# Performance work log

Measured on AMD Instinct MI355X. Metric: run time of the kernel, lower is better.

Reference implementation:

```python
import jax, jax.numpy as jnp
import numpy as np

NUM_HEADS = 16


def _qdq(x):
    """Symmetric int8 fake-quant along the last axis (per-token for
    activations, per-output-channel for [out,in] weights). Equivalent math to
    int8 GEMM with dynamic scales: (x_q @ w_q.T) * sx * sw == qdq(x) @ qdq(w).T."""
    s = jnp.maximum(jnp.max(jnp.abs(x), axis=-1, keepdims=True) / 127.0, 1e-8)
    return jnp.clip(jnp.round(x / s), -127.0, 127.0) * s


def setup_inputs() -> dict:
    key = jax.random.key(0)
    ks = jax.random.split(key, 8)
    B, N, M, D = 2, 4096, 512, 2048
    w_std = 0.02
    return {
        "x": jax.random.normal(ks[0], (B, N, D), jnp.float32),
        "cond": jax.random.normal(ks[1], (B, M, D), jnp.float32),
        "wq": jax.random.normal(ks[2], (D, D), jnp.float32) * w_std,
        "bq": jax.random.normal(ks[3], (D,), jnp.float32) * w_std,
        "wkv": jax.random.normal(ks[4], (2 * D, D), jnp.float32) * w_std,
        "bkv": jax.random.normal(ks[5], (2 * D,), jnp.float32) * w_std,
        "wp": jax.random.normal(ks[6], (D, D), jnp.float32) * w_std,
        "bp": jax.random.normal(ks[7], (D,), jnp.float32) * w_std,
    }


def reference(x, cond, wq, bq, wkv, bkv, wp, bp):
    B, N, C = x.shape
    M = cond.shape[1]
    H = NUM_HEADS
    Dh = C // H

    # W8A8 dynamic-scale q projection (per-token act quant, per-channel weight quant)
    q = _qdq(x) @ _qdq(wq).T + bq                      # [B,N,C]
    # fp16-style kv projection
    kv = cond @ wkv.T + bkv                            # [B,M,2C]
    k, v = jnp.split(kv, 2, axis=-1)                   # view(...,2,H,Dh).unbind(2)

    q = q.reshape(B, N, H, Dh)
    k = k.reshape(B, M, H, Dh)
    v = v.reshape(B, M, H, Dh)

    scale = 1.0 / np.sqrt(Dh)
    attn = jax.nn.softmax(jnp.einsum('bnhd,bmhd->bhnm', q, k) * scale, axis=-1)
    o = jnp.einsum('bhnm,bmhd->bnhd', attn, v).reshape(B, N, C)

    # fused quant_sum (per-token requant of attention output) + W8A8 proj
    out = _qdq(o) @ _qdq(wp).T + bp                    # [B,N,C]
    return out
```

## Files before the change

kernel.cpp:

```cpp
#include <hip/hip_runtime.h>
#include <cstdint>
#include <cstddef>


typedef __bf16 bf16_t;
typedef __bf16 bf16x8 __attribute__((ext_vector_type(8)));
typedef float f32x4 __attribute__((ext_vector_type(4)));

__device__ __forceinline__ void gld16(void* lds, const void* g) {
    __builtin_amdgcn_global_load_lds(
        (__attribute__((address_space(1))) uint32_t*)(uintptr_t)g,
        (__attribute__((address_space(3))) uint32_t*)(uint32_t)(uintptr_t)lds,
        16, 0, 0);
}

__device__ __forceinline__ void load8(const float* p, int i, float* v) {
    const float4* p4 = (const float4*)p;
    float4 a = p4[2 * i], b = p4[2 * i + 1];
    v[0] = a.x; v[1] = a.y; v[2] = a.z; v[3] = a.w;
    v[4] = b.x; v[5] = b.y; v[6] = b.z; v[7] = b.w;
}
__device__ __forceinline__ void load8(const bf16_t* p, int i, float* v) {
    bf16x8 t = ((const bf16x8*)p)[i];
#pragma unroll
    for (int j = 0; j < 8; ++j) v[j] = (float)t[j];
}

template <int QUANT, typename T>
__global__ __launch_bounds__(256) void rowpack(const T* __restrict__ in,
                                               bf16_t* __restrict__ out, int K) {
    const int tid = threadIdx.x;
    const size_t row = blockIdx.x;
    const T* rp = in + row * (size_t)K;
    const int n8 = K >> 3;
    float scale = 1.0f;
    if (QUANT) {
        float m = 0.f;
        for (int i = tid; i < n8; i += 256) {
            float v[8];
            load8(rp, i, v);
#pragma unroll
            for (int j = 0; j < 8; ++j) m = fmaxf(m, fabsf(v[j]));
        }
        __shared__ float red[256];
        red[tid] = m;
        __syncthreads();
        for (int s = 128; s > 0; s >>= 1) {
            if (tid < s) red[tid] = fmaxf(red[tid], red[tid + s]);
            __syncthreads();
        }
        scale = fmaxf(red[0] * (1.0f / 127.0f), 1e-8f);
    }
    const int KT = K >> 5;
    const int p = (int)(row >> 7), c = ((int)row >> 4) & 7, lm = (int)row & 15;
    for (int i = tid; i < n8; i += 256) {
        const int col = i << 3;
        const int kt = col >> 5, quad = (col >> 3) & 3;
        float v[8];
        load8(rp, i, v);
        bf16x8 o8;
#pragma unroll
        for (int j = 0; j < 8; ++j) {
            float q = v[j];
            if (QUANT) {
                q = rintf(q / scale);
                q = fminf(127.f, fmaxf(-127.f, q)) * scale;
            }
            o8[j] = (bf16_t)q;
        }
        const size_t dst = ((size_t)(p * KT + kt) * 8 + c) * 512 + (quad * 16 + lm) * 8;
        *(bf16x8*)(out + dst) = o8;
    }
}

template <int MODE>
__device__ __forceinline__ void epi_store(void* C, int N, int row, int col, float v) {
    if (MODE == 1) {
        ((float*)C)[(size_t)row * N + col] = v;
    } else if (MODE == 0) {
        const int b = row >> 12, n = row & 4095;
        const int h = col >> 7, d = col & 127;
        const int p = n >> 6, mt = (n >> 4) & 3, lmq = n & 15;
        const int kq = d >> 5, qq = (d >> 3) & 3, jq = d & 7;
        const size_t idx = (((size_t)(b * 16 + h) * 64 + p) * 16 + kq * 4 + mt) * 512 +
                           (qq * 16 + lmq) * 8 + jq;
        ((bf16_t*)C)[idx] = (bf16_t)v;
    } else {
        const int b = row >> 9, m = row & 511;
        const int half = col >> 11, h = (col >> 7) & 15, d = col & 127;
        const int t8 = m >> 6;
        bf16_t* out = (bf16_t*)C;
        if (half == 0) {
            const int nt = (m >> 4) & 3, lmk = m & 15;
            const int kc = d >> 5, qk = (d >> 3) & 3, jk = d & 7;
            const size_t idx = (((size_t)(b * 16 + h) * 8 + t8) * 16 + kc * 4 + nt) * 512 +
                               (qk * 16 + lmk) * 8 + jk;
            out[idx] = (bf16_t)v;
        } else {
            const int kv2 = (m >> 5) & 1, qv = (m >> 3) & 3, jv = m & 7;
            const int ntv = d >> 4, lmv = d & 15;
            const size_t idx = 2097152 +
                (((size_t)(b * 16 + h) * 8 + t8) * 16 + kv2 * 8 + ntv) * 512 +
                (qv * 16 + lmv) * 8 + jv;
            out[idx] = (bf16_t)v;
        }
    }
}

__device__ __forceinline__ void stage_tile256(const bf16_t* __restrict__ A,
                                              const bf16_t* __restrict__ B,
                                              bf16_t* sa, bf16_t* sb,
                                              int pa, int pb, int KT, int t,
                                              int w, int l) {
#pragma unroll
    for (int it = 0; it < 4; ++it) {
        const int ci = w * 4 + it;
        const int h = ci >> 4, kt2 = (ci >> 3) & 1, c = ci & 7;
        const size_t ga = (((size_t)(pa + h) * KT + (2 * t + kt2)) * 8 + c) * 512 + l * 8;
        const size_t gb = (((size_t)(pb + h) * KT + (2 * t + kt2)) * 8 + c) * 512 + l * 8;
        gld16(sa + ci * 512, A + ga);
        gld16(sb + ci * 512, B + gb);
    }
}

template <int MODE>
__global__ __launch_bounds__(512, 1) void gemm_pk8(const bf16_t* __restrict__ A,
                                                   const bf16_t* __restrict__ B,
                                                   const float* __restrict__ bias,
                                                   void* __restrict__ C,
                                                   int N, int K) {
    __shared__ __align__(16) bf16_t sA[2][16384];
    __shared__ __align__(16) bf16_t sB[2][16384];

    const int tid = threadIdx.x;
    const int l = tid & 63, w = tid >> 6;
    const int lm = l & 15, quad = l >> 4;
    const int wm = w & 1, wn = w >> 1;

    const int nwg = gridDim.x;
    const int bid = blockIdx.x;
    const int s = (bid & 7) * (nwg >> 3) + (bid >> 3);
    const int bx = s & 7, by = s >> 3;

    const int KT = K >> 5;
    const int NT = K >> 6;
    const int pa = by * 2, pb = bx * 2;

    stage_tile256(A, B, sA[0], sB[0], pa, pb, KT, 0, w, l);
    __builtin_amdgcn_sched_barrier(0);
    stage_tile256(A, B, sA[1], sB[1], pa, pb, KT, 1, w, l);
    asm volatile("s_waitcnt vmcnt(8)" ::: "memory");
    __builtin_amdgcn_s_barrier();

    f32x4 acc[8][4] = {};

    for (int t = 0; t < NT; ++t) {
        const bf16_t* sa = sA[t & 1];
        const bf16_t* sb = sB[t & 1];
        bf16x8 bfr[4][2];
        bf16x8 af[2][2];

#pragma unroll
        for (int j = 0; j < 4; ++j)
#pragma unroll
            for (int k2 = 0; k2 < 2; ++k2)
                bfr[j][k2] = *(const bf16x8*)(
                    sb + ((((wn >> 1) * 2 + k2) * 8 + (wn & 1) * 4 + j) * 512) + l * 8);
#pragma unroll
        for (int ii = 0; ii < 2; ++ii)
#pragma unroll
            for (int k2 = 0; k2 < 2; ++k2)
                af[ii][k2] = *(const bf16x8*)(sa + (((wm * 2 + k2) * 8 + ii) * 512) + l * 8);
        __builtin_amdgcn_s_barrier();
        asm volatile("s_waitcnt lgkmcnt(0)" ::: "memory");
        __builtin_amdgcn_sched_barrier(0);
        __builtin_amdgcn_s_setprio(1);
#pragma unroll
        for (int ii = 0; ii < 2; ++ii)
#pragma unroll
            for (int j = 0; j < 4; ++j)
#pragma unroll
                for (int k2 = 0; k2 < 2; ++k2)
                    acc[ii][j] = __builtin_amdgcn_mfma_f32_16x16x32_bf16(
                        af[ii][k2], bfr[j][k2], acc[ii][j], 0, 0, 0);
        __builtin_amdgcn_s_setprio(0);
        __builtin_amdgcn_s_barrier();

#pragma unroll
        for (int q = 1; q <= 2; ++q) {
#pragma unroll
            for (int ii = 0; ii < 2; ++ii)
#pragma unroll
                for (int k2 = 0; k2 < 2; ++k2)
                    af[ii][k2] = *(const bf16x8*)(
                        sa + (((wm * 2 + k2) * 8 + (q * 2 + ii)) * 512) + l * 8);
            __builtin_amdgcn_s_barrier();
            asm volatile("s_waitcnt lgkmcnt(0)" ::: "memory");
            __builtin_amdgcn_sched_barrier(0);
            __builtin_amdgcn_s_setprio(1);
#pragma unroll
            for (int ii = 0; ii < 2; ++ii)
#pragma unroll
                for (int j = 0; j < 4; ++j)
#pragma unroll
                    for (int k2 = 0; k2 < 2; ++k2)
                        acc[q * 2 + ii][j] = __builtin_amdgcn_mfma_f32_16x16x32_bf16(
                            af[ii][k2], bfr[j][k2], acc[q * 2 + ii][j], 0, 0, 0);
            __builtin_amdgcn_s_setprio(0);
            __builtin_amdgcn_s_barrier();
        }

#pragma unroll
        for (int ii = 0; ii < 2; ++ii)
#pragma unroll
            for (int k2 = 0; k2 < 2; ++k2)
                af[ii][k2] = *(const bf16x8*)(
                    sa + (((wm * 2 + k2) * 8 + (6 + ii)) * 512) + l * 8);
        asm volatile("s_waitcnt lgkmcnt(0)" ::: "memory");
        __builtin_amdgcn_s_barrier();
        if (t + 2 < NT)
            stage_tile256(A, B, sA[t & 1], sB[t & 1], pa, pb, KT, t + 2, w, l);
        __builtin_amdgcn_sched_barrier(0);
        __builtin_amdgcn_s_setprio(1);
#pragma unroll
        for (int ii = 0; ii < 2; ++ii)
#pragma unroll
            for (int j = 0; j < 4; ++j)
#pragma unroll
                for (int k2 = 0; k2 < 2; ++k2)
                    acc[6 + ii][j] = __builtin_amdgcn_mfma_f32_16x16x32_bf16(
                        af[ii][k2], bfr[j][k2], acc[6 + ii][j], 0, 0, 0);
        __builtin_amdgcn_s_setprio(0);
        if (t + 2 < NT)
            asm volatile("s_waitcnt vmcnt(8)" ::: "memory");
        else
            asm volatile("s_waitcnt vmcnt(0)" ::: "memory");
        __builtin_amdgcn_s_barrier();
    }

#pragma unroll
    for (int i = 0; i < 8; ++i) {
#pragma unroll
        for (int j = 0; j < 4; ++j) {
            const int col = bx * 256 + wn * 64 + j * 16 + lm;
            const float bv = bias[col];
#pragma unroll
            for (int r = 0; r < 4; ++r) {
                const int row = by * 256 + wm * 128 + i * 16 + quad * 4 + r;
                epi_store<MODE>(C, N, row, col, acc[i][j][r] + bv);
            }
        }
    }
}

__global__ __launch_bounds__(256) void gemm_kv(const bf16_t* __restrict__ A,
                                               const bf16_t* __restrict__ B,
                                               const float* __restrict__ bias,
                                               bf16_t* __restrict__ C,
                                               int N, int K) {
    __shared__ __align__(16) bf16_t sA[4096];
    __shared__ __align__(16) bf16_t sB[8192];

    const int tid = threadIdx.x;
    const int l = tid & 63, w = tid >> 6;
    const int lm = l & 15, quad = l >> 4;
    const int wm = w & 1, wn = w >> 1;
    const int KT = K >> 5;
    const int p = blockIdx.y >> 1, hh = blockIdx.y & 1;
    const size_t aPan = (size_t)p * KT * 8 * 512;
    const size_t bBase = (size_t)blockIdx.x * KT * 8 * 512;

    f32x4 acc[2][4] = {};
    const int NIT = K >> 6;
    for (int kt = 0; kt < NIT; ++kt) {
        __syncthreads();
#pragma unroll
        for (int it = 0; it < 2; ++it) {
            const int lc = it * 4 + w;
            const int s = lc >> 2, cc = lc & 3;
            gld16(sA + lc * 512,
                  A + aPan + ((size_t)(kt * 2 + s) * 8 + hh * 4 + cc) * 512 + l * 8);
        }
#pragma unroll
        for (int it = 0; it < 4; ++it) {
            const int lc = it * 4 + w;
            gld16(sB + lc * 512, B + bBase + ((size_t)kt * 16 + lc) * 512 + l * 8);
        }
        __syncthreads();
#pragma unroll
        for (int s = 0; s < 2; ++s) {
            bf16x8 af[2], bfr[4];
#pragma unroll
            for (int i = 0; i < 2; ++i)
                af[i] = *(const bf16x8*)(sA + (s * 4 + wm * 2 + i) * 512 + l * 8);
#pragma unroll
            for (int j = 0; j < 4; ++j)
                bfr[j] = *(const bf16x8*)(sB + (s * 8 + wn * 4 + j) * 512 + l * 8);
#pragma unroll
            for (int i = 0; i < 2; ++i)
#pragma unroll
                for (int j = 0; j < 4; ++j)
                    acc[i][j] =
                        __builtin_amdgcn_mfma_f32_16x16x32_bf16(af[i], bfr[j], acc[i][j], 0, 0, 0);
        }
    }
#pragma unroll
    for (int i = 0; i < 2; ++i) {
#pragma unroll
        for (int j = 0; j < 4; ++j) {
            const int col = blockIdx.x * 128 + wn * 64 + j * 16 + lm;
            const float bv = bias[col];
#pragma unroll
            for (int r = 0; r < 4; ++r) {
                const int row = blockIdx.y * 64 + wm * 32 + i * 16 + quad * 4 + r;
                epi_store<2>(C, N, row, col, acc[i][j][r] + bv);
            }
        }
    }
}

__global__ __launch_bounds__(256, 2) void attn64(const bf16_t* __restrict__ qpk,
                                                 const bf16_t* __restrict__ kvpk,
                                                 bf16_t* __restrict__ o) {
    constexpr float SCALE = 0.08838834764831845f;
    __shared__ __align__(16) bf16_t sQP[8192];
    __shared__ __align__(16) bf16_t sKV[16384];
    __shared__ float redM[4][64];
    __shared__ float redS[4][64];

    const int tid = threadIdx.x;
    const int l = tid & 63, w = tid >> 6;
    const int lm = l & 15, quad = l >> 4;
    const int b = blockIdx.z, h = blockIdx.y;
    const int p = blockIdx.x;
    const int bh = b * 16 + h;
    const size_t qbase = ((size_t)bh * 64 + p) * 8192;
    const size_t kbase = (size_t)bh * 65536;
    const size_t vbase = 2097152 + (size_t)bh * 65536;

#pragma unroll
    for (int it = 0; it < 4; ++it) {
        const int c = it * 4 + w;
        gld16(sQP + c * 512, qpk + qbase + (size_t)c * 512 + l * 8);
    }

    f32x4 sfr[8][4] = {};
#pragma unroll
    for (int g = 0; g < 4; ++g) {
        __syncthreads();
#pragma unroll
        for (int it = 0; it < 8; ++it) {
            const int c = it * 4 + w;
            gld16(sKV + c * 512, kvpk + kbase + ((size_t)g * 32 + c) * 512 + l * 8);
        }
        __syncthreads();
#pragma unroll
        for (int kc = 0; kc < 4; ++kc) {
#pragma unroll
            for (int kk = 0; kk < 2; ++kk) {
                bf16x8 bb = *(const bf16x8*)(sKV + (kk * 16 + kc * 4 + w) * 512 + l * 8);
#pragma unroll
                for (int mt = 0; mt < 4; ++mt) {
                    bf16x8 aa = *(const bf16x8*)(sQP + (kc * 4 + mt) * 512 + l * 8);
                    sfr[g * 2 + kk][mt] =
                        __builtin_amdgcn_mfma_f32_16x16x32_bf16(aa, bb, sfr[g * 2 + kk][mt], 0, 0, 0);
                }
            }
        }
    }

    float inv[4][4];
    {
        float mymax[4][4];
#pragma unroll
        for (int mt = 0; mt < 4; ++mt)
#pragma unroll
            for (int r = 0; r < 4; ++r) {
                float m = -3.0e38f;
#pragma unroll
                for (int t8 = 0; t8 < 8; ++t8) m = fmaxf(m, sfr[t8][mt][r]);
                m = fmaxf(m, __shfl_xor(m, 1));
                m = fmaxf(m, __shfl_xor(m, 2));
                m = fmaxf(m, __shfl_xor(m, 4));
                m = fmaxf(m, __shfl_xor(m, 8));
                mymax[mt][r] = m;
            }
        if (lm == 0) {
#pragma unroll
            for (int mt = 0; mt < 4; ++mt)
#pragma unroll
                for (int r = 0; r < 4; ++r)
                    redM[w][mt * 16 + quad * 4 + r] = mymax[mt][r];
        }
        __syncthreads();
#pragma unroll
        for (int mt = 0; mt < 4; ++mt)
#pragma unroll
            for (int r = 0; r < 4; ++r) {
                const int row = mt * 16 + quad * 4 + r;
                const float M =
                    fmaxf(fmaxf(redM[0][row], redM[1][row]), fmaxf(redM[2][row], redM[3][row])) *
                    SCALE;
                float s = 0.f;
#pragma unroll
                for (int t8 = 0; t8 < 8; ++t8) {
                    const float pe = __expf(sfr[t8][mt][r] * SCALE - M);
                    sfr[t8][mt][r] = pe;
                    s += pe;
                }
                s += __shfl_xor(s, 1);
                s += __shfl_xor(s, 2);
                s += __shfl_xor(s, 4);
                s += __shfl_xor(s, 8);
                if (lm == 0) redS[w][row] = s;
            }
        __syncthreads();
#pragma unroll
        for (int mt = 0; mt < 4; ++mt)
#pragma unroll
            for (int r = 0; r < 4; ++r) {
                const int row = mt * 16 + quad * 4 + r;
                inv[mt][r] = 1.f / (redS[0][row] + redS[1][row] + redS[2][row] + redS[3][row]);
            }
    }

    f32x4 oc[4][2] = {};
    const int ktd = w >> 1;
    const int quadd = (w & 1) * 2 + (lm >> 3);
    const int jd = lm & 7;
#pragma unroll
    for (int g = 0; g < 4; ++g) {
        __syncthreads();
#pragma unroll
        for (int kk = 0; kk < 2; ++kk)
#pragma unroll
            for (int mt = 0; mt < 4; ++mt)
#pragma unroll
                for (int r = 0; r < 4; ++r)
                    sQP[(mt * 4 + kk * 2 + ktd) * 512 + (quadd * 16 + quad * 4 + r) * 8 + jd] =
                        (bf16_t)sfr[g * 2 + kk][mt][r];
#pragma unroll
        for (int it = 0; it < 8; ++it) {
            const int c = it * 4 + w;
            gld16(sKV + c * 512, kvpk + vbase + ((size_t)g * 32 + c) * 512 + l * 8);
        }
        __syncthreads();
#pragma unroll
        for (int kvf = 0; kvf < 4; ++kvf) {
            const int kk = kvf >> 1, kv2 = kvf & 1;
            bf16x8 aa[4];
#pragma unroll
            for (int mt = 0; mt < 4; ++mt)
                aa[mt] = *(const bf16x8*)(sQP + (mt * 4 + kvf) * 512 + l * 8);
#pragma unroll
            for (int ni = 0; ni < 2; ++ni) {
                bf16x8 bb =
                    *(const bf16x8*)(sKV + (kk * 16 + kv2 * 8 + w * 2 + ni) * 512 + l * 8);
#pragma unroll
                for (int mt = 0; mt < 4; ++mt)
                    oc[mt][ni] =
                        __builtin_amdgcn_mfma_f32_16x16x32_bf16(aa[mt], bb, oc[mt][ni], 0, 0, 0);
            }
        }
    }

#pragma unroll
    for (int mt = 0; mt < 4; ++mt)
#pragma unroll
        for (int ni = 0; ni < 2; ++ni)
#pragma unroll
            for (int r = 0; r < 4; ++r) {
                const int row = mt * 16 + quad * 4 + r;
                const int d = w * 32 + ni * 16 + lm;
                o[((size_t)b * 4096 + p * 64 + row) * 2048 + h * 128 + d] =
                    (bf16_t)(oc[mt][ni][r] * inv[mt][r]);
            }
}

extern "C" void kernel_launch(void* const* d_in, const int* in_sizes, int n_in,
                              void* d_out, int out_size, void* d_ws, size_t ws_size,
                              hipStream_t stream) {
    (void)in_sizes; (void)n_in; (void)out_size; (void)ws_size;
    const float* x    = (const float*)d_in[0];
    const float* cond = (const float*)d_in[1];
    const float* wq   = (const float*)d_in[2];
    const float* bq   = (const float*)d_in[3];
    const float* wkv  = (const float*)d_in[4];
    const float* bkv  = (const float*)d_in[5];
    const float* wp   = (const float*)d_in[6];
    const float* bp   = (const float*)d_in[7];

    const size_t MB = 1ull << 20;
    uint8_t* ws = (uint8_t*)d_ws;
    bf16_t* qxpk   = (bf16_t*)(ws + 0);
    bf16_t* qpk    = (bf16_t*)(ws + 32 * MB);
    bf16_t* wqpk   = (bf16_t*)(ws + 64 * MB);
    bf16_t* wkvpk  = (bf16_t*)(ws + 72 * MB);
    bf16_t* wppk   = (bf16_t*)(ws + 88 * MB);
    bf16_t* condpk = (bf16_t*)(ws + 96 * MB);
    bf16_t* kvpk   = (bf16_t*)(ws + 100 * MB);
    bf16_t* o_nat  = qxpk;
    bf16_t* opk    = qpk;

    dim3 blk(256);
    rowpack<1, float><<<8192, blk, 0, stream>>>(x, qxpk, 2048);
    rowpack<1, float><<<2048, blk, 0, stream>>>(wq, wqpk, 2048);
    rowpack<1, float><<<2048, blk, 0, stream>>>(wp, wppk, 2048);
    rowpack<0, float><<<1024, blk, 0, stream>>>(cond, condpk, 2048);
    rowpack<0, float><<<4096, blk, 0, stream>>>(wkv, wkvpk, 2048);
    gemm_pk8<0><<<dim3(256), dim3(512), 0, stream>>>(qxpk, wqpk, bq, qpk, 2048, 2048);
    gemm_kv<<<dim3(32, 16), blk, 0, stream>>>(condpk, wkvpk, bkv, kvpk, 4096, 2048);
    attn64<<<dim3(64, 16, 2), blk, 0, stream>>>(qpk, kvpk, o_nat);
    rowpack<1, bf16_t><<<8192, blk, 0, stream>>>(o_nat, opk, 2048);
    gemm_pk8<1><<<dim3(256), dim3(512), 0, stream>>>(opk, wppk, bp, (float*)d_out, 2048, 2048);
}
```

Baseline: 511.1 us.

## Double-buffer K and V tiles in attention kernel with async prefetch

```diff
diff --git a/kernel.cpp b/kernel.cpp
--- a/kernel.cpp
+++ b/kernel.cpp
@@ -343,30 +343,48 @@
         const int c = it * 4 + w;
         gld16(sQP + c * 512, qpk + qbase + (size_t)c * 512 + l * 8);
     }
+#pragma unroll
+    for (int it = 0; it < 4; ++it) {
+        const int c = it * 4 + w;
+        gld16(sKV + c * 512, kvpk + kbase + (size_t)c * 512 + l * 8);
+    }
 
     f32x4 sfr[8][4] = {};
 #pragma unroll
-    for (int g = 0; g < 4; ++g) {
-        __syncthreads();
-#pragma unroll
-        for (int it = 0; it < 8; ++it) {
-            const int c = it * 4 + w;
-            gld16(sKV + c * 512, kvpk + kbase + ((size_t)g * 32 + c) * 512 + l * 8);
-        }
-        __syncthreads();
+    for (int sg = 0; sg < 8; ++sg) {
+        if (sg < 7) {
+            bf16_t* kn = sKV + (((sg + 1) & 1) << 13);
+#pragma unroll
+            for (int it = 0; it < 4; ++it) {
+                const int c = it * 4 + w;
+                gld16(kn + c * 512, kvpk + kbase + ((size_t)(sg + 1) * 16 + c) * 512 + l * 8);
+            }
+            asm volatile("s_waitcnt vmcnt(4)" ::: "memory");
+        } else {
+            asm volatile("s_waitcnt vmcnt(0)" ::: "memory");
+        }
+        __builtin_amdgcn_s_barrier();
+        const bf16_t* kb = sKV + ((sg & 1) << 13);
+        __builtin_amdgcn_s_setprio(1);
 #pragma unroll
         for (int kc = 0; kc < 4; ++kc) {
-#pragma unroll
-            for (int kk = 0; kk < 2; ++kk) {
-                bf16x8 bb = *(const bf16x8*)(sKV + (kk * 16 + kc * 4 + w) * 512 + l * 8);
-#pragma unroll
-                for (int mt = 0; mt < 4; ++mt) {
-                    bf16x8 aa = *(const bf16x8*)(sQP + (kc * 4 + mt) * 512 + l * 8);
-                    sfr[g * 2 + kk][mt] =
-                        __builtin_amdgcn_mfma_f32_16x16x32_bf16(aa, bb, sfr[g * 2 + kk][mt], 0, 0, 0);
-                }
-            }
-        }
+            bf16x8 bb = *(const bf16x8*)(kb + (kc * 4 + w) * 512 + l * 8);
+#pragma unroll
+            for (int mt = 0; mt < 4; ++mt) {
+                bf16x8 aa = *(const bf16x8*)(sQP + (kc * 4 + mt) * 512 + l * 8);
+                sfr[sg][mt] =
+                    __builtin_amdgcn_mfma_f32_16x16x32_bf16(aa, bb, sfr[sg][mt], 0, 0, 0);
+            }
+        }
+        __builtin_amdgcn_s_setprio(0);
+        asm volatile("s_waitcnt lgkmcnt(0)" ::: "memory");
+        __builtin_amdgcn_s_barrier();
+    }
+
+#pragma unroll
+    for (int it = 0; it < 4; ++it) {
+        const int c = it * 4 + w;
+        gld16(sKV + c * 512, kvpk + vbase + (size_t)c * 512 + l * 8);
     }
 
     float inv[4][4];
@@ -392,7 +410,8 @@
                 for (int r = 0; r < 4; ++r)
                     redM[w][mt * 16 + quad * 4 + r] = mymax[mt][r];
         }
-        __syncthreads();
+        asm volatile("s_waitcnt lgkmcnt(0)" ::: "memory");
+        __builtin_amdgcn_s_barrier();
 #pragma unroll
         for (int mt = 0; mt < 4; ++mt)
 #pragma unroll
@@ -414,7 +433,8 @@
                 s += __shfl_xor(s, 8);
                 if (lm == 0) redS[w][row] = s;
             }
-        __syncthreads();
+        asm volatile("s_waitcnt lgkmcnt(0)" ::: "memory");
+        __builtin_amdgcn_s_barrier();
 #pragma unroll
         for (int mt = 0; mt < 4; ++mt)
 #pragma unroll
@@ -424,45 +444,58 @@
             }
     }
 
+    const int kvh = w >> 1;
+    const int quadp = (w & 1) * 2 + (lm >> 3);
+    const int jd = lm & 7;
+#define PWRITE(sg_) do {                                                          \
+    const int r8_ = ((sg_) & 1) * 8;                                              \
+    _Pragma("unroll") for (int mt = 0; mt < 4; ++mt)                              \
+    _Pragma("unroll") for (int r = 0; r < 4; ++r)                                 \
+        sQP[(r8_ + mt * 2 + kvh) * 512 + (quadp * 16 + quad * 4 + r) * 8 + jd] =  \
+            (bf16_t)sfr[sg_][mt][r];                                              \
+} while (0)
+
     f32x4 oc[4][2] = {};
-    const int ktd = w >> 1;
-    const int quadd = (w & 1) * 2 + (lm >> 3);
-    const int jd = lm & 7;
-#pragma unroll
-    for (int g = 0; g < 4; ++g) {
-        __syncthreads();
-#pragma unroll
-        for (int kk = 0; kk < 2; ++kk)
+    PWRITE(0);
+#pragma unroll
+    for (int sg = 0; sg < 8; ++sg) {
+        if (sg < 7) {
+            bf16_t* vn = sKV + (((sg + 1) & 1) << 13);
+#pragma unroll
+            for (int it = 0; it < 4; ++it) {
+                const int c = it * 4 + w;
+                gld16(vn + c * 512, kvpk + vbase + ((size_t)(sg + 1) * 16 + c) * 512 + l * 8);
+            }
+            PWRITE(sg + 1);
+            asm volatile("s_waitcnt vmcnt(4)" ::: "memory");
+        } else {
+            asm volatile("s_waitcnt vmcnt(0)" ::: "memory");
+        }
+        asm volatile("s_waitcnt lgkmcnt(0)" ::: "memory");
+        __builtin_amdgcn_s_barrier();
+        const bf16_t* vb = sKV + ((sg & 1) << 13);
+        const bf16_t* pb = sQP + ((sg & 1) << 12);
+        __builtin_amdgcn_s_setprio(1);
+#pragma unroll
+        for (int kvf2 = 0; kvf2 < 2; ++kvf2) {
+            bf16x8 aa[4];
 #pragma unroll
             for (int mt = 0; mt < 4; ++mt)
-#pragma unroll
-                for (int r = 0; r < 4; ++r)
-                    sQP[(mt * 4 + kk * 2 + ktd) * 512 + (quadd * 16 + quad * 4 + r) * 8 + jd] =
-                        (bf16_t)sfr[g * 2 + kk][mt][r];
-#pragma unroll
-        for (int it = 0; it < 8; ++it) {
-            const int c = it * 4 + w;
-            gld16(sKV + c * 512, kvpk + vbase + ((size_t)g * 32 + c) * 512 + l * 8);
-        }
-        __syncthreads();
-#pragma unroll
-        for (int kvf = 0; kvf < 4; ++kvf) {
-            const int kk = kvf >> 1, kv2 = kvf & 1;
-            bf16x8 aa[4];
-#pragma unroll
-            for (int mt = 0; mt < 4; ++mt)
-                aa[mt] = *(const bf16x8*)(sQP + (mt * 4 + kvf) * 512 + l * 8);
+                aa[mt] = *(const bf16x8*)(pb + (mt * 2 + kvf2) * 512 + l * 8);
 #pragma unroll
             for (int ni = 0; ni < 2; ++ni) {
-                bf16x8 bb =
-                    *(const bf16x8*)(sKV + (kk * 16 + kv2 * 8 + w * 2 + ni) * 512 + l * 8);
+                bf16x8 bb = *(const bf16x8*)(vb + (kvf2 * 8 + w * 2 + ni) * 512 + l * 8);
 #pragma unroll
                 for (int mt = 0; mt < 4; ++mt)
                     oc[mt][ni] =
                         __builtin_amdgcn_mfma_f32_16x16x32_bf16(aa[mt], bb, oc[mt][ni], 0, 0, 0);
             }
         }
-    }
+        __builtin_amdgcn_s_setprio(0);
+        asm volatile("s_waitcnt lgkmcnt(0)" ::: "memory");
+        __builtin_amdgcn_s_barrier();
+    }
+#undef PWRITE
 
 #pragma unroll
     for (int mt = 0; mt < 4; ++mt)
```

New measurement: 513.0 us. No clear change (+0.4%).
